# Kernel optimization log

Measured on AMD Instinct MI355X. Metric: run time of the kernel, lower is better.

The kernel has to match this reference:

```python
import jax, jax.numpy as jnp
import numpy as np

B, N, D = 2, 2048, 1024
H, WS = 16, 128  # num_heads, window_size
DH = D // H
HALF = WS // 2  # window is [i-HALF, i+HALF] inclusive -> 129 keys interior


def setup_inputs() -> dict:
    key = jax.random.key(0)
    ks = jax.random.split(key, 5)
    return {
        "x": jax.random.normal(ks[0], (B, N, D), dtype=jnp.float32),
        "Wqkv": jax.random.normal(ks[1], (D, 3 * D), dtype=jnp.float32) * 0.02,
        "bqkv": jax.random.normal(ks[2], (3 * D,), dtype=jnp.float32) * 0.02,
        "Wout": jax.random.normal(ks[3], (D, D), dtype=jnp.float32) * 0.02,
        "bout": jax.random.normal(ks[4], (D,), dtype=jnp.float32) * 0.02,
    }


def reference(x, Wqkv, bqkv, Wout, bout):
    b, n, d = x.shape
    scale = DH ** -0.5
    qkv = x @ Wqkv + bqkv  # [b, n, 3d]
    q, k, v = jnp.split(qkv, 3, axis=-1)
    # [b, n, d] -> [b, h, n, dh]
    def heads(t):
        return t.reshape(b, n, H, DH).transpose(0, 2, 1, 3)
    q, k, v = heads(q), heads(k), heads(v)
    scores = jnp.einsum("bhid,bhjd->bhij", q, k) * scale  # [b, h, n, n]
    # per-token window [max(0,i-HALF), min(n,i+HALF+1)) == |i-j| <= HALF
    idx = jnp.arange(n)
    band = jnp.abs(idx[:, None] - idx[None, :]) <= HALF  # [n, n]
    neg = jnp.asarray(jnp.finfo(scores.dtype).min, scores.dtype)
    scores = jnp.where(band[None, None], scores, neg)
    attn = jax.nn.softmax(scores, axis=-1)
    out = jnp.einsum("bhij,bhjd->bhid", attn, v)  # [b, h, n, dh]
    out = out.transpose(0, 2, 1, 3).reshape(b, n, d)
    return out @ Wout + bout
```

## Files before the change

### kernel.cpp

```cpp
#include <hip/hip_runtime.h>
#include <hip/hip_bf16.h>
#include <cstdint>
#include <cstddef>

#define BB 2
#define NN 2048
#define DD 1024
#define HH 16
#define DHH 64
#define SCALE 0.125f

typedef _Float16 f16x8 __attribute__((ext_vector_type(8)));
typedef _Float16 f16x4 __attribute__((ext_vector_type(4)));
typedef float f32x4 __attribute__((ext_vector_type(4)));

#define AS1(p) ((__attribute__((address_space(1))) void*)(p))
#define AS3(p) ((__attribute__((address_space(3))) void*)(p))

__global__ __launch_bounds__(256) void cvt_f32_to_f16(const float* __restrict__ in,
                                                      _Float16* __restrict__ out, int n) {
    int i = (blockIdx.x * 256 + threadIdx.x) * 8;
    if (i + 8 <= n) {
        f32x4 a = *(const f32x4*)(in + i);
        f32x4 b = *(const f32x4*)(in + i + 4);
        f16x8 o;
        o[0] = (_Float16)a[0]; o[1] = (_Float16)a[1]; o[2] = (_Float16)a[2]; o[3] = (_Float16)a[3];
        o[4] = (_Float16)b[0]; o[5] = (_Float16)b[1]; o[6] = (_Float16)b[2]; o[7] = (_Float16)b[3];
        *(f16x8*)(out + i) = o;
    }
}

__global__ __launch_bounds__(256) void transpose_cvt(const float* __restrict__ in,
                                                     _Float16* __restrict__ out, int R, int C) {
    __shared__ float tile[32][33];
    int tx = threadIdx.x & 31, ty = threadIdx.x >> 5;
    int r0 = blockIdx.y * 32, c0 = blockIdx.x * 32;
#pragma unroll
    for (int i = 0; i < 32; i += 8)
        tile[ty + i][tx] = in[(size_t)(r0 + ty + i) * C + (c0 + tx)];
    __syncthreads();
#pragma unroll
    for (int i = 0; i < 32; i += 8)
        out[(size_t)(c0 + ty + i) * R + (r0 + tx)] = (_Float16)tile[tx][ty + i];
}

__global__ __launch_bounds__(256) void gemm_f16_bt(const _Float16* __restrict__ A,
                                                   const _Float16* __restrict__ Bt,
                                                   const float* __restrict__ bias,
                                                   _Float16* __restrict__ Ch,
                                                   float* __restrict__ Cf,
                                                   int M, int N, int K) {
    __shared__ __align__(16) _Float16 As[128 * 64];
    __shared__ __align__(16) _Float16 Bs[128 * 64];
    int tid = threadIdx.x;
    int wave = tid >> 6, lane = tid & 63;
    int bm = blockIdx.y * 128, bn = blockIdx.x * 128;
    int wm = (wave >> 1) * 64, wn = (wave & 1) * 64;
    int lhi = lane >> 4, llo = lane & 15;

    f32x4 acc[4][4] = {};

    int srow = wave * 32 + (lane >> 3);
    int scol = (((lane & 7) ^ (lane >> 3))) * 8;
    const _Float16* gA = A + (size_t)(bm + srow) * K + scol;
    const _Float16* gB = Bt + (size_t)(bn + srow) * K + scol;
    _Float16* lA = As + wave * 2048 + lane * 8;
    _Float16* lB = Bs + wave * 2048 + lane * 8;

    for (int k0 = 0; k0 < K; k0 += 64) {
        __syncthreads();
#pragma unroll
        for (int p = 0; p < 4; ++p) {
            __builtin_amdgcn_global_load_lds(AS1(gA + (size_t)p * 8 * K + k0), AS3(lA + p * 512), 16, 0, 0);
            __builtin_amdgcn_global_load_lds(AS1(gB + (size_t)p * 8 * K + k0), AS3(lB + p * 512), 16, 0, 0);
        }
        __syncthreads();

#pragma unroll
        for (int ks = 0; ks < 2; ++ks) {
            f16x8 af[4], bf[4];
            int cc = ks * 4 + lhi;
            int swzA = ((cc ^ (llo & 7)) * 8);
#pragma unroll
            for (int mt = 0; mt < 4; ++mt)
                af[mt] = *(const f16x8*)(As + (wm + mt * 16 + llo) * 64 + swzA);
#pragma unroll
            for (int nt = 0; nt < 4; ++nt)
                bf[nt] = *(const f16x8*)(Bs + (wn + nt * 16 + llo) * 64 + swzA);
#pragma unroll
            for (int mt = 0; mt < 4; ++mt)
#pragma unroll
                for (int nt = 0; nt < 4; ++nt)
                    acc[mt][nt] = __builtin_amdgcn_mfma_f32_16x16x32_f16(af[mt], bf[nt], acc[mt][nt], 0, 0, 0);
        }
    }

#pragma unroll
    for (int nt = 0; nt < 4; ++nt) {
        int col = bn + wn + nt * 16 + llo;
        float bv = bias[col];
#pragma unroll
        for (int mt = 0; mt < 4; ++mt) {
#pragma unroll
            for (int r = 0; r < 4; ++r) {
                int row = bm + wm + mt * 16 + lhi * 4 + r;
                float v = acc[mt][nt][r] + bv;
                if (Ch) Ch[(size_t)row * N + col] = (_Float16)v;
                else    Cf[(size_t)row * N + col] = v;
            }
        }
    }
}

#define KP 72
#define PP 200
#define VP 200
__global__ __launch_bounds__(256) void local_attn(const _Float16* __restrict__ qkv,
                                                  _Float16* __restrict__ outh) {
    __shared__ __align__(16) _Float16 Ks[192 * KP];
    __shared__ __align__(16) _Float16 Ps[64 * PP];
    __shared__ __align__(16) _Float16 Vt[64 * VP];
    int tid = threadIdx.x;
    int i0 = blockIdx.x * 64;
    int h = blockIdx.y, b = blockIdx.z;
    const size_t rs = 3 * DD;
    const _Float16* base = qkv + (size_t)(b * NN) * rs + h * DHH;

    for (int u = tid; u < 1536; u += 256) {
        int s = u >> 3, d8c = u & 7, d8 = d8c * 8;
        int j = i0 - 64 + s;
        f16x8 kv = {0,0,0,0,0,0,0,0}, vv = {0,0,0,0,0,0,0,0};
        if (j >= 0 && j < NN) {
            const _Float16* p = base + (size_t)j * rs + d8;
            kv = *(const f16x8*)(p + DD);
            vv = *(const f16x8*)(p + 2 * DD);
        }
        *(f16x8*)(Ks + s * KP + d8) = kv;
#pragma unroll
        for (int i = 0; i < 8; ++i) {
            int t = (i + d8c) & 7;
            Vt[(d8 + t) * VP + s] = vv[t];
        }
    }
    for (int u = tid; u < 512; u += 256) {
        int r = u >> 3, d8 = (u & 7) * 8;
        f16x8 qv = *(const f16x8*)(base + (size_t)(i0 + r) * rs + d8);
        *(f16x8*)(Ps + r * PP + d8) = qv;
    }
    __syncthreads();

    int wave = tid >> 6, lane = tid & 63;
    int llo = lane & 15, lhi = lane >> 4;
    int qrow = wave * 16 + llo;
    int qi = i0 + qrow;

    f16x8 qf0 = *(const f16x8*)(Ps + qrow * PP + lhi * 8);
    f16x8 qf1 = *(const f16x8*)(Ps + qrow * PP + 32 + lhi * 8);
    float sc[12][4];
#pragma unroll
    for (int mt = 0; mt < 12; ++mt) {
        f16x8 kf0 = *(const f16x8*)(Ks + (mt * 16 + llo) * KP + lhi * 8);
        f16x8 kf1 = *(const f16x8*)(Ks + (mt * 16 + llo) * KP + 32 + lhi * 8);
        f32x4 a = {0.f, 0.f, 0.f, 0.f};
        a = __builtin_amdgcn_mfma_f32_16x16x32_f16(kf0, qf0, a, 0, 0, 0);
        a = __builtin_amdgcn_mfma_f32_16x16x32_f16(kf1, qf1, a, 0, 0, 0);
#pragma unroll
        for (int r = 0; r < 4; ++r) sc[mt][r] = a[r];
    }

    float m = -1e30f;
#pragma unroll
    for (int mt = 0; mt < 12; ++mt)
#pragma unroll
        for (int r = 0; r < 4; ++r) {
            int sidx = mt * 16 + lhi * 4 + r;
            int j = i0 - 64 + sidx;
            int dj = j - qi;
            bool valid = (j >= 0) && (j < NN) && (dj <= 64) && (dj >= -64);
            float v = valid ? sc[mt][r] * SCALE : -1e30f;
            sc[mt][r] = v;
            m = fmaxf(m, v);
        }
    m = fmaxf(m, __shfl_xor(m, 16, 64));
    m = fmaxf(m, __shfl_xor(m, 32, 64));
    float l = 0.f;
#pragma unroll
    for (int mt = 0; mt < 12; ++mt)
#pragma unroll
        for (int r = 0; r < 4; ++r) {
            float e = __expf(sc[mt][r] - m);
            sc[mt][r] = e;
            l += e;
        }
    l += __shfl_xor(l, 16, 64);
    l += __shfl_xor(l, 32, 64);
    float invl = 1.f / l;

#pragma unroll
    for (int mt = 0; mt < 12; ++mt) {
        f16x4 pv;
#pragma unroll
        for (int r = 0; r < 4; ++r) pv[r] = (_Float16)(sc[mt][r] * invl);
        *(f16x4*)(Ps + qrow * PP + mt * 16 + lhi * 4) = pv;
    }
    __asm__ volatile("s_waitcnt lgkmcnt(0)" ::: "memory");

    f32x4 oacc[4] = {};
#pragma unroll
    for (int ks = 0; ks < 6; ++ks) {
        f16x8 pf = *(const f16x8*)(Ps + (wave * 16 + llo) * PP + ks * 32 + lhi * 8);
#pragma unroll
        for (int nt = 0; nt < 4; ++nt) {
            f16x8 vf = *(const f16x8*)(Vt + (nt * 16 + llo) * VP + ks * 32 + lhi * 8);
            oacc[nt] = __builtin_amdgcn_mfma_f32_16x16x32_f16(pf, vf, oacc[nt], 0, 0, 0);
        }
    }

    _Float16* orow = outh + (size_t)(b * NN) * DD + h * DHH;
#pragma unroll
    for (int nt = 0; nt < 4; ++nt)
#pragma unroll
        for (int r = 0; r < 4; ++r) {
            int q = wave * 16 + lhi * 4 + r;
            int d = nt * 16 + llo;
            orow[(size_t)(i0 + q) * DD + d] = (_Float16)oacc[nt][r];
        }
}

extern "C" void kernel_launch(void* const* d_in, const int* in_sizes, int n_in,
                              void* d_out, int out_size, void* d_ws, size_t ws_size,
                              hipStream_t stream) {
    const float* x    = (const float*)d_in[0];
    const float* Wqkv = (const float*)d_in[1];
    const float* bqkv = (const float*)d_in[2];
    const float* Wout = (const float*)d_in[3];
    const float* bout = (const float*)d_in[4];
    float* out = (float*)d_out;

    char* ws = (char*)d_ws;
    _Float16* x_h    = (_Float16*)(ws);
    _Float16* Wqkv_t = (_Float16*)(ws + (size_t)8  * 1024 * 1024);
    _Float16* Wout_t = (_Float16*)(ws + (size_t)14 * 1024 * 1024);
    _Float16* qkv_h  = (_Float16*)(ws + (size_t)16 * 1024 * 1024);
    _Float16* attn_h = (_Float16*)(ws + (size_t)40 * 1024 * 1024);

    int M = BB * NN;

    cvt_f32_to_f16<<<(M * DD) / (256 * 8), 256, 0, stream>>>(x, x_h, M * DD);
    transpose_cvt<<<dim3((3 * DD) / 32, DD / 32), 256, 0, stream>>>(Wqkv, Wqkv_t, DD, 3 * DD);
    transpose_cvt<<<dim3(DD / 32, DD / 32), 256, 0, stream>>>(Wout, Wout_t, DD, DD);

    gemm_f16_bt<<<dim3((3 * DD) / 128, M / 128), 256, 0, stream>>>(
        x_h, Wqkv_t, bqkv, qkv_h, nullptr, M, 3 * DD, DD);

    local_attn<<<dim3(NN / 64, HH, BB), 256, 0, stream>>>(qkv_h, attn_h);

    gemm_f16_bt<<<dim3(DD / 128, M / 128), 256, 0, stream>>>(
        attn_h, Wout_t, bout, nullptr, out, M, DD, DD);
}
```

Before: 165.8 us.

## Fuse prep kernels, use 64-row tiles for output GEMM, async-load K in attention

The f32-to-f16 conversion of x and the two weight transpose-converts are merged into one `prep` launch, which removes two kernel launches. The GEMM is templated on its M tile; the output projection now uses 64-row tiles, doubling the block count to fill more CUs. In local attention, K is staged into LDS with `global_load_lds` using an XOR-swizzled unpadded layout, and Q is read straight into registers instead of through LDS. The K load no longer bounds-checks, so edge blocks read neighbouring workspace memory; those scores are masked out afterwards, but it depends on the masking being applied.

```diff
diff --git a/kernel.cpp b/kernel.cpp
--- a/kernel.cpp
+++ b/kernel.cpp
@@ -17,78 +17,85 @@
 #define AS1(p) ((__attribute__((address_space(1))) void*)(p))
 #define AS3(p) ((__attribute__((address_space(3))) void*)(p))
 
-__global__ __launch_bounds__(256) void cvt_f32_to_f16(const float* __restrict__ in,
-                                                      _Float16* __restrict__ out, int n) {
-    int i = (blockIdx.x * 256 + threadIdx.x) * 8;
-    if (i + 8 <= n) {
-        f32x4 a = *(const f32x4*)(in + i);
-        f32x4 b = *(const f32x4*)(in + i + 4);
+__global__ __launch_bounds__(256) void prep(const float* __restrict__ x, _Float16* __restrict__ x_h,
+                                            const float* __restrict__ Wqkv, _Float16* __restrict__ Wqkv_t,
+                                            const float* __restrict__ Wout, _Float16* __restrict__ Wout_t) {
+    __shared__ float tile[32][33];
+    int bx = blockIdx.x, tid = threadIdx.x;
+    if (bx < 2048) {
+        int i = bx * 2048 + tid * 8;
+        f32x4 a = *(const f32x4*)(x + i);
+        f32x4 b = *(const f32x4*)(x + i + 4);
         f16x8 o;
         o[0] = (_Float16)a[0]; o[1] = (_Float16)a[1]; o[2] = (_Float16)a[2]; o[3] = (_Float16)a[3];
         o[4] = (_Float16)b[0]; o[5] = (_Float16)b[1]; o[6] = (_Float16)b[2]; o[7] = (_Float16)b[3];
-        *(f16x8*)(out + i) = o;
-    }
-}
-
-__global__ __launch_bounds__(256) void transpose_cvt(const float* __restrict__ in,
-                                                     _Float16* __restrict__ out, int R, int C) {
-    __shared__ float tile[32][33];
-    int tx = threadIdx.x & 31, ty = threadIdx.x >> 5;
-    int r0 = blockIdx.y * 32, c0 = blockIdx.x * 32;
+        *(f16x8*)(x_h + i) = o;
+        return;
+    }
+    const float* in; _Float16* out; int C, tc, tr;
+    if (bx < 5120) { int t = bx - 2048; C = 3 * DD; in = Wqkv; out = Wqkv_t; tc = t % 96; tr = t / 96; }
+    else           { int t = bx - 5120; C = DD;     in = Wout; out = Wout_t; tc = t % 32; tr = t / 32; }
+    int R = DD;
+    int txx = tid & 31, ty = tid >> 5;
+    int r0 = tr * 32, c0 = tc * 32;
 #pragma unroll
     for (int i = 0; i < 32; i += 8)
-        tile[ty + i][tx] = in[(size_t)(r0 + ty + i) * C + (c0 + tx)];
+        tile[ty + i][txx] = in[(size_t)(r0 + ty + i) * C + (c0 + txx)];
     __syncthreads();
 #pragma unroll
     for (int i = 0; i < 32; i += 8)
-        out[(size_t)(c0 + ty + i) * R + (r0 + tx)] = (_Float16)tile[tx][ty + i];
-}
-
+        out[(size_t)(c0 + ty + i) * R + (r0 + txx)] = (_Float16)tile[txx][ty + i];
+}
+
+template <int BM>
 __global__ __launch_bounds__(256) void gemm_f16_bt(const _Float16* __restrict__ A,
                                                    const _Float16* __restrict__ Bt,
                                                    const float* __restrict__ bias,
                                                    _Float16* __restrict__ Ch,
                                                    float* __restrict__ Cf,
                                                    int M, int N, int K) {
-    __shared__ __align__(16) _Float16 As[128 * 64];
+    constexpr int MT = BM / 32;
+    constexpr int AP = BM / 32;
+    __shared__ __align__(16) _Float16 As[BM * 64];
     __shared__ __align__(16) _Float16 Bs[128 * 64];
     int tid = threadIdx.x;
     int wave = tid >> 6, lane = tid & 63;
-    int bm = blockIdx.y * 128, bn = blockIdx.x * 128;
-    int wm = (wave >> 1) * 64, wn = (wave & 1) * 64;
+    int bm = blockIdx.y * BM, bn = blockIdx.x * 128;
+    int wm = (wave >> 1) * (BM / 2), wn = (wave & 1) * 64;
     int lhi = lane >> 4, llo = lane & 15;
 
-    f32x4 acc[4][4] = {};
-
-    int srow = wave * 32 + (lane >> 3);
-    int scol = (((lane & 7) ^ (lane >> 3))) * 8;
-    const _Float16* gA = A + (size_t)(bm + srow) * K + scol;
-    const _Float16* gB = Bt + (size_t)(bn + srow) * K + scol;
-    _Float16* lA = As + wave * 2048 + lane * 8;
+    f32x4 acc[MT][4] = {};
+
+    int srowA = wave * (BM / 4) + (lane >> 3);
+    int srowB = wave * 32 + (lane >> 3);
+    int scol = ((lane & 7) ^ (lane >> 3)) * 8;
+    const _Float16* gA = A + (size_t)(bm + srowA) * K + scol;
+    const _Float16* gB = Bt + (size_t)(bn + srowB) * K + scol;
+    _Float16* lA = As + wave * (AP * 512) + lane * 8;
     _Float16* lB = Bs + wave * 2048 + lane * 8;
 
     for (int k0 = 0; k0 < K; k0 += 64) {
         __syncthreads();
 #pragma unroll
-        for (int p = 0; p < 4; ++p) {
+        for (int p = 0; p < AP; ++p)
             __builtin_amdgcn_global_load_lds(AS1(gA + (size_t)p * 8 * K + k0), AS3(lA + p * 512), 16, 0, 0);
+#pragma unroll
+        for (int p = 0; p < 4; ++p)
             __builtin_amdgcn_global_load_lds(AS1(gB + (size_t)p * 8 * K + k0), AS3(lB + p * 512), 16, 0, 0);
-        }
         __syncthreads();
 
 #pragma unroll
         for (int ks = 0; ks < 2; ++ks) {
-            f16x8 af[4], bf[4];
-            int cc = ks * 4 + lhi;
-            int swzA = ((cc ^ (llo & 7)) * 8);
-#pragma unroll
-            for (int mt = 0; mt < 4; ++mt)
-                af[mt] = *(const f16x8*)(As + (wm + mt * 16 + llo) * 64 + swzA);
+            f16x8 af[MT], bf[4];
+            int swz = (((ks * 4 + lhi) ^ (llo & 7)) * 8);
+#pragma unroll
+            for (int mt = 0; mt < MT; ++mt)
+                af[mt] = *(const f16x8*)(As + (wm + mt * 16 + llo) * 64 + swz);
 #pragma unroll
             for (int nt = 0; nt < 4; ++nt)
-                bf[nt] = *(const f16x8*)(Bs + (wn + nt * 16 + llo) * 64 + swzA);
-#pragma unroll
-            for (int mt = 0; mt < 4; ++mt)
+                bf[nt] = *(const f16x8*)(Bs + (wn + nt * 16 + llo) * 64 + swz);
+#pragma unroll
+            for (int mt = 0; mt < MT; ++mt)
 #pragma unroll
                 for (int nt = 0; nt < 4; ++nt)
                     acc[mt][nt] = __builtin_amdgcn_mfma_f32_16x16x32_f16(af[mt], bf[nt], acc[mt][nt], 0, 0, 0);
@@ -100,7 +107,7 @@
         int col = bn + wn + nt * 16 + llo;
         float bv = bias[col];
 #pragma unroll
-        for (int mt = 0; mt < 4; ++mt) {
+        for (int mt = 0; mt < MT; ++mt) {
 #pragma unroll
             for (int r = 0; r < 4; ++r) {
                 int row = bm + wm + mt * 16 + lhi * 4 + r;
@@ -112,7 +119,7 @@
     }
 }
 
-#define KP 72
+#define KP 64
 #define PP 200
 #define VP 200
 __global__ __launch_bounds__(256) void local_attn(const _Float16* __restrict__ qkv,
@@ -123,44 +130,50 @@
     int tid = threadIdx.x;
     int i0 = blockIdx.x * 64;
     int h = blockIdx.y, b = blockIdx.z;
-    const size_t rs = 3 * DD;
-    const _Float16* base = qkv + (size_t)(b * NN) * rs + h * DHH;
+    const ptrdiff_t rs = 3 * DD;
+    const _Float16* base = qkv + (ptrdiff_t)(b * NN) * rs + h * DHH;
+
+    int wave = tid >> 6, lane = tid & 63;
+    int llo = lane & 15, lhi = lane >> 4;
+
+    {
+        int srow = lane >> 3;
+        int chunk = ((lane & 7) ^ (lane >> 3)) * 8;
+#pragma unroll
+        for (int q = 0; q < 6; ++q) {
+            int p = wave * 6 + q;
+            int j = i0 - 64 + p * 8 + srow;
+            const _Float16* g = base + (ptrdiff_t)j * rs + DD + chunk;
+            __builtin_amdgcn_global_load_lds(AS1(g), AS3(Ks + p * 512 + lane * 8), 16, 0, 0);
+        }
+    }
 
     for (int u = tid; u < 1536; u += 256) {
         int s = u >> 3, d8c = u & 7, d8 = d8c * 8;
         int j = i0 - 64 + s;
-        f16x8 kv = {0,0,0,0,0,0,0,0}, vv = {0,0,0,0,0,0,0,0};
-        if (j >= 0 && j < NN) {
-            const _Float16* p = base + (size_t)j * rs + d8;
-            kv = *(const f16x8*)(p + DD);
-            vv = *(const f16x8*)(p + 2 * DD);
-        }
-        *(f16x8*)(Ks + s * KP + d8) = kv;
+        f16x8 vv = {0,0,0,0,0,0,0,0};
+        if (j >= 0 && j < NN)
+            vv = *(const f16x8*)(base + (ptrdiff_t)j * rs + 2 * DD + d8);
 #pragma unroll
         for (int i = 0; i < 8; ++i) {
             int t = (i + d8c) & 7;
             Vt[(d8 + t) * VP + s] = vv[t];
         }
     }
-    for (int u = tid; u < 512; u += 256) {
-        int r = u >> 3, d8 = (u & 7) * 8;
-        f16x8 qv = *(const f16x8*)(base + (size_t)(i0 + r) * rs + d8);
-        *(f16x8*)(Ps + r * PP + d8) = qv;
-    }
-    __syncthreads();
-
-    int wave = tid >> 6, lane = tid & 63;
-    int llo = lane & 15, lhi = lane >> 4;
+
     int qrow = wave * 16 + llo;
     int qi = i0 + qrow;
-
-    f16x8 qf0 = *(const f16x8*)(Ps + qrow * PP + lhi * 8);
-    f16x8 qf1 = *(const f16x8*)(Ps + qrow * PP + 32 + lhi * 8);
+    const _Float16* qp = base + (ptrdiff_t)qi * rs;
+    f16x8 qf0 = *(const f16x8*)(qp + lhi * 8);
+    f16x8 qf1 = *(const f16x8*)(qp + 32 + lhi * 8);
+    __syncthreads();
+
     float sc[12][4];
 #pragma unroll
     for (int mt = 0; mt < 12; ++mt) {
-        f16x8 kf0 = *(const f16x8*)(Ks + (mt * 16 + llo) * KP + lhi * 8);
-        f16x8 kf1 = *(const f16x8*)(Ks + (mt * 16 + llo) * KP + 32 + lhi * 8);
+        const _Float16* kr = Ks + (mt * 16 + llo) * 64;
+        f16x8 kf0 = *(const f16x8*)(kr + ((lhi ^ (llo & 7)) * 8));
+        f16x8 kf1 = *(const f16x8*)(kr + (((lhi + 4) ^ (llo & 7)) * 8));
         f32x4 a = {0.f, 0.f, 0.f, 0.f};
         a = __builtin_amdgcn_mfma_f32_16x16x32_f16(kf0, qf0, a, 0, 0, 0);
         a = __builtin_amdgcn_mfma_f32_16x16x32_f16(kf1, qf1, a, 0, 0, 0);
@@ -246,15 +259,13 @@
 
     int M = BB * NN;
 
-    cvt_f32_to_f16<<<(M * DD) / (256 * 8), 256, 0, stream>>>(x, x_h, M * DD);
-    transpose_cvt<<<dim3((3 * DD) / 32, DD / 32), 256, 0, stream>>>(Wqkv, Wqkv_t, DD, 3 * DD);
-    transpose_cvt<<<dim3(DD / 32, DD / 32), 256, 0, stream>>>(Wout, Wout_t, DD, DD);
-
-    gemm_f16_bt<<<dim3((3 * DD) / 128, M / 128), 256, 0, stream>>>(
+    prep<<<6144, 256, 0, stream>>>(x, x_h, Wqkv, Wqkv_t, Wout, Wout_t);
+
+    gemm_f16_bt<128><<<dim3((3 * DD) / 128, M / 128), 256, 0, stream>>>(
         x_h, Wqkv_t, bqkv, qkv_h, nullptr, M, 3 * DD, DD);
 
     local_attn<<<dim3(NN / 64, HH, BB), 256, 0, stream>>>(qkv_h, attn_h);
 
-    gemm_f16_bt<<<dim3(DD / 128, M / 128), 256, 0, stream>>>(
+    gemm_f16_bt<64><<<dim3(DD / 128, M / 64), 256, 0, stream>>>(
         attn_h, Wout_t, bout, nullptr, out, M, DD, DD);
 }
```

After: 159.5 us. 3.8% less time.
